# Optimization experiments

Hardware: AMD Instinct MI355X
Metric: run time of the kernel (lower is better)

The kernel has to match this reference:

```python
import jax, jax.numpy as jnp
import numpy as np

B, N, D = 8192, 50, 64


def setup_inputs() -> dict:
    key = jax.random.key(0)
    k1, k2, k3 = jax.random.split(key, 3)
    F = jax.random.normal(k1, (B, N, D), dtype=jnp.float32)
    # xavier_normal for square DxD linear: std = sqrt(2/(D+D)) = 1/sqrt(D)
    std = 1.0 / np.sqrt(D)
    K_w = jax.random.normal(k2, (D, D), dtype=jnp.float32) * std
    Q_w = jax.random.normal(k3, (D, D), dtype=jnp.float32) * std
    return {"F": F, "K_w": K_w, "Q_w": Q_w}


def reference(F, K_w, Q_w):
    # K(F): Linear with weight K_w (torch convention: x @ W^T)
    KF = jnp.einsum('bnd,ed->bne', F, K_w)          # [B,N,D]
    # S = F @ K(F)^T
    S = jnp.einsum('bnd,bmd->bnm', F, KF)           # [B,N,N]
    # out[b,n,d] = sum_m S[b,n,m] * F[b,n,d] * F[b,m,d]
    #            = F[b,n,d] * (S @ F)[b,n,d]   (algebraic fusion of the
    #              bnd,bmd->bnmd outer product + weighted sum over m)
    out = F * jnp.einsum('bnm,bmd->bnd', S, F)      # [B,N,D]
    # residual branch: Q(F)
    out = out + jnp.einsum('bnd,ed->bne', F, Q_w)
    return out
```

## Files before the change

### kernel.cpp

```cpp
#include <hip/hip_runtime.h>

typedef __attribute__((ext_vector_type(8))) short s16x8;
typedef __attribute__((ext_vector_type(4))) short s16x4;
typedef __attribute__((ext_vector_type(4))) float f32x4;

#define ST 72
#define NB 8
#define MFMA __builtin_amdgcn_mfma_f32_16x16x32_bf16

__device__ __forceinline__ short f2bf(float f) {
    unsigned u = __builtin_bit_cast(unsigned, f);
    u += 0x7FFFu + ((u >> 16) & 1u);
    return (short)(u >> 16);
}
__device__ __forceinline__ s16x8 cvt8(f32x4 a, f32x4 b) {
    s16x8 r = { f2bf(a.x), f2bf(a.y), f2bf(a.z), f2bf(a.w),
                f2bf(b.x), f2bf(b.y), f2bf(b.z), f2bf(b.w) };
    return r;
}

__global__ __launch_bounds__(256, 4) void sam3e_v2(
    const float* __restrict__ F, const float* __restrict__ Kw,
    const float* __restrict__ Qw, float* __restrict__ out)
{
    __shared__ __align__(16) short sKw[64 * ST];
    __shared__ __align__(16) short sQw[64 * ST];
    __shared__ __align__(16) short sAT[64 * ST];
    __shared__ __align__(16) short sKS[64 * ST];

    const int tid  = threadIdx.x;
    const int w    = tid >> 6;
    const int lane = tid & 63;
    const int col  = lane & 15;
    const int q    = lane >> 4;

    {
        const int e  = tid & 63;
        const int dg = tid >> 6;
        const f32x4* Kv = (const f32x4*)(Kw + e * 64 + dg * 16);
        const f32x4* Qv = (const f32x4*)(Qw + e * 64 + dg * 16);
        #pragma unroll
        for (int k = 0; k < 4; ++k) {
            f32x4 kv = Kv[k], qv = Qv[k];
            s16x4 hk = { f2bf(kv.x), f2bf(kv.y), f2bf(kv.z), f2bf(kv.w) };
            s16x4 hq = { f2bf(qv.x), f2bf(qv.y), f2bf(qv.z), f2bf(qv.w) };
            *(s16x4*)&sKw[e * ST + dg * 16 + k * 4] = hk;
            *(s16x4*)&sQw[e * ST + dg * 16 + k * 4] = hq;
        }
    }

    const int sn  = tid & 63;
    const int sdg = tid >> 6;
    const f32x4 z4 = {0.f, 0.f, 0.f, 0.f};

    int b = blockIdx.x * NB;
    f32x4 pf0 = z4, pf1 = z4, pf2 = z4, pf3 = z4;
    if (sn < 50) {
        const f32x4* Fr = (const f32x4*)(F + (size_t)b * 3200 + sn * 64 + sdg * 16);
        pf0 = Fr[0]; pf1 = Fr[1]; pf2 = Fr[2]; pf3 = Fr[3];
    }

    for (int it = 0; it < NB; ++it, ++b) {
        const float* Fb = F   + (size_t)b * 3200;
        float*       Ob = out + (size_t)b * 3200;

        __syncthreads();

        {
            const int d0 = sdg * 16;
            short h[16] = { f2bf(pf0.x), f2bf(pf0.y), f2bf(pf0.z), f2bf(pf0.w),
                            f2bf(pf1.x), f2bf(pf1.y), f2bf(pf1.z), f2bf(pf1.w),
                            f2bf(pf2.x), f2bf(pf2.y), f2bf(pf2.z), f2bf(pf2.w),
                            f2bf(pf3.x), f2bf(pf3.y), f2bf(pf3.z), f2bf(pf3.w) };
            #pragma unroll
            for (int i = 0; i < 16; ++i) sAT[(d0 + i) * ST + sn] = h[i];
        }

        s16x8 a0, a1;
        {
            const int row = 16 * w + col;
            f32x4 v0 = z4, v1 = z4, v2 = z4, v3 = z4;
            if (row < 50) {
                const f32x4* Fr = (const f32x4*)(Fb + row * 64);
                v0 = Fr[2 * q]; v1 = Fr[2 * q + 1];
                v2 = Fr[8 + 2 * q]; v3 = Fr[8 + 2 * q + 1];
            }
            a0 = cvt8(v0, v1); a1 = cvt8(v2, v3);
        }

        #pragma unroll
        for (int nt = 0; nt < 4; ++nt) {
            const short* yb = &sKw[(16 * nt + col) * ST + 8 * q];
            f32x4 acc = {0.f, 0.f, 0.f, 0.f};
            acc = MFMA(a0, *(const s16x8*)yb,        acc, 0, 0, 0);
            acc = MFMA(a1, *(const s16x8*)(yb + 32), acc, 0, 0, 0);
            #pragma unroll
            for (int r = 0; r < 4; ++r)
                sKS[(16 * w + 4 * q + r) * ST + 16 * nt + col] = f2bf(acc[r]);
        }
        __syncthreads();

        f32x4 S[4];
        #pragma unroll
        for (int nt = 0; nt < 4; ++nt) {
            const short* yb = &sKS[(16 * nt + col) * ST + 8 * q];
            f32x4 acc = {0.f, 0.f, 0.f, 0.f};
            acc = MFMA(a0, *(const s16x8*)yb,        acc, 0, 0, 0);
            acc = MFMA(a1, *(const s16x8*)(yb + 32), acc, 0, 0, 0);
            S[nt] = acc;
        }

        if (it + 1 < NB && sn < 50) {
            const f32x4* Fr = (const f32x4*)(Fb + 3200 + sn * 64 + sdg * 16);
            pf0 = Fr[0]; pf1 = Fr[1]; pf2 = Fr[2]; pf3 = Fr[3];
        }

        __syncthreads();
        #pragma unroll
        for (int nt = 0; nt < 4; ++nt)
            #pragma unroll
            for (int r = 0; r < 4; ++r)
                sKS[(16 * w + 4 * q + r) * ST + 16 * nt + col] = f2bf(S[nt][r]);
        __syncthreads();

        const short* sb = &sKS[(16 * w + col) * ST + 8 * q];
        s16x8 s0 = *(const s16x8*)sb;
        s16x8 s1 = *(const s16x8*)(sb + 32);
        #pragma unroll
        for (int nt = 0; nt < 4; ++nt) {
            const short* tb = &sAT[(16 * nt + col) * ST + 8 * q];
            const short* qb = &sQw[(16 * nt + col) * ST + 8 * q];
            f32x4 t  = {0.f, 0.f, 0.f, 0.f};
            f32x4 qa = {0.f, 0.f, 0.f, 0.f};
            t  = MFMA(s0, *(const s16x8*)tb,        t,  0, 0, 0);
            t  = MFMA(s1, *(const s16x8*)(tb + 32), t,  0, 0, 0);
            qa = MFMA(a0, *(const s16x8*)qb,        qa, 0, 0, 0);
            qa = MFMA(a1, *(const s16x8*)(qb + 32), qa, 0, 0, 0);
            #pragma unroll
            for (int r = 0; r < 4; ++r) {
                const int n = 16 * w + 4 * q + r;
                if (n < 50) {
                    const int idx = n * 64 + 16 * nt + col;
                    Ob[idx] = Fb[idx] * t[r] + qa[r];
                }
            }
        }
    }
}

extern "C" void kernel_launch(void* const* d_in, const int* in_sizes, int n_in,
                              void* d_out, int out_size, void* d_ws, size_t ws_size,
                              hipStream_t stream) {
    const float* F  = (const float*)d_in[0];
    const float* Kw = (const float*)d_in[1];
    const float* Qw = (const float*)d_in[2];
    float* out = (float*)d_out;
    sam3e_v2<<<8192 / NB, 256, 0, stream>>>(F, Kw, Qw, out);
}
```

Baseline: 237.9 us.

## Give each wavefront its own batch items with private LDS and register-held weights

Restructures the kernel so each wavefront processes whole batch items independently, using a private LDS slice per wave and removing all block-level barriers. K and Q weights are converted to bf16 and kept in registers instead of LDS, the MFMA operand order is transposed so outputs come out as float4-vectorized stores, and the transposed-F LDS layout uses an XOR swizzle to reduce bank conflicts. It drops the previous register prefetch of the next batch item and lowers the occupancy hint, trading barrier stalls for higher register pressure and less latency hiding.

Measured after the change: 232.5 us. -2.2%, faster.

```diff
diff --git a/kernel.cpp b/kernel.cpp
--- a/kernel.cpp
+++ b/kernel.cpp
@@ -5,7 +5,6 @@
 typedef __attribute__((ext_vector_type(4))) float f32x4;
 
 #define ST 72
-#define NB 8
 #define MFMA __builtin_amdgcn_mfma_f32_16x16x32_bf16
 
 __device__ __forceinline__ short f2bf(float f) {
@@ -18,15 +17,16 @@
                 f2bf(b.x), f2bf(b.y), f2bf(b.z), f2bf(b.w) };
     return r;
 }
+__device__ __forceinline__ s16x4 cvt4(f32x4 a) {
+    s16x4 r = { f2bf(a.x), f2bf(a.y), f2bf(a.z), f2bf(a.w) };
+    return r;
+}
 
-__global__ __launch_bounds__(256, 4) void sam3e_v2(
+__global__ __launch_bounds__(256, 2) void sam3e_v3(
     const float* __restrict__ F, const float* __restrict__ Kw,
     const float* __restrict__ Qw, float* __restrict__ out)
 {
-    __shared__ __align__(16) short sKw[64 * ST];
-    __shared__ __align__(16) short sQw[64 * ST];
-    __shared__ __align__(16) short sAT[64 * ST];
-    __shared__ __align__(16) short sKS[64 * ST];
+    __shared__ __align__(16) short lds[4][2][64 * ST];
 
     const int tid  = threadIdx.x;
     const int w    = tid >> 6;
@@ -34,114 +34,110 @@
     const int col  = lane & 15;
     const int q    = lane >> 4;
 
-    {
-        const int e  = tid & 63;
-        const int dg = tid >> 6;
-        const f32x4* Kv = (const f32x4*)(Kw + e * 64 + dg * 16);
-        const f32x4* Qv = (const f32x4*)(Qw + e * 64 + dg * 16);
+    short* sAT = &lds[w][0][0];
+    short* sKS = &lds[w][1][0];
+
+    s16x8 kX[4][2], qX[4][2];
+    #pragma unroll
+    for (int t = 0; t < 4; ++t) {
+        const float* kr = Kw + (16*t + col)*64 + 8*q;
+        const float* qr = Qw + (16*t + col)*64 + 8*q;
         #pragma unroll
-        for (int k = 0; k < 4; ++k) {
-            f32x4 kv = Kv[k], qv = Qv[k];
-            s16x4 hk = { f2bf(kv.x), f2bf(kv.y), f2bf(kv.z), f2bf(kv.w) };
-            s16x4 hq = { f2bf(qv.x), f2bf(qv.y), f2bf(qv.z), f2bf(qv.w) };
-            *(s16x4*)&sKw[e * ST + dg * 16 + k * 4] = hk;
-            *(s16x4*)&sQw[e * ST + dg * 16 + k * 4] = hq;
+        for (int h = 0; h < 2; ++h) {
+            kX[t][h] = cvt8(*(const f32x4*)(kr + 32*h), *(const f32x4*)(kr + 32*h + 4));
+            qX[t][h] = cvt8(*(const f32x4*)(qr + 32*h), *(const f32x4*)(qr + 32*h + 4));
         }
     }
 
-    const int sn  = tid & 63;
-    const int sdg = tid >> 6;
     const f32x4 z4 = {0.f, 0.f, 0.f, 0.f};
+    const int gw = blockIdx.x * 4 + w;
 
-    int b = blockIdx.x * NB;
-    f32x4 pf0 = z4, pf1 = z4, pf2 = z4, pf3 = z4;
-    if (sn < 50) {
-        const f32x4* Fr = (const f32x4*)(F + (size_t)b * 3200 + sn * 64 + sdg * 16);
-        pf0 = Fr[0]; pf1 = Fr[1]; pf2 = Fr[2]; pf3 = Fr[3];
-    }
-
-    for (int it = 0; it < NB; ++it, ++b) {
+    #pragma unroll 1
+    for (int it = 0; it < 4; ++it) {
+        const int b = gw * 4 + it;
         const float* Fb = F   + (size_t)b * 3200;
         float*       Ob = out + (size_t)b * 3200;
 
-        __syncthreads();
-
-        {
-            const int d0 = sdg * 16;
-            short h[16] = { f2bf(pf0.x), f2bf(pf0.y), f2bf(pf0.z), f2bf(pf0.w),
-                            f2bf(pf1.x), f2bf(pf1.y), f2bf(pf1.z), f2bf(pf1.w),
-                            f2bf(pf2.x), f2bf(pf2.y), f2bf(pf2.z), f2bf(pf2.w),
-                            f2bf(pf3.x), f2bf(pf3.y), f2bf(pf3.z), f2bf(pf3.w) };
+        s16x8 aX[4][2];
+        #pragma unroll
+        for (int t = 0; t < 4; ++t) {
+            const int n = 16*t + col;
+            f32x4 v0 = z4, v1 = z4, v2 = z4, v3 = z4;
+            if (n < 50) {
+                const f32x4* Fr = (const f32x4*)(Fb + n*64 + 8*q);
+                v0 = Fr[0]; v1 = Fr[1]; v2 = Fr[8]; v3 = Fr[9];
+            }
+            aX[t][0] = cvt8(v0, v1);
+            aX[t][1] = cvt8(v2, v3);
+            const int mc = n ^ (q << 3);
+            short h0[8] = { f2bf(v0.x), f2bf(v0.y), f2bf(v0.z), f2bf(v0.w),
+                            f2bf(v1.x), f2bf(v1.y), f2bf(v1.z), f2bf(v1.w) };
+            short h1[8] = { f2bf(v2.x), f2bf(v2.y), f2bf(v2.z), f2bf(v2.w),
+                            f2bf(v3.x), f2bf(v3.y), f2bf(v3.z), f2bf(v3.w) };
             #pragma unroll
-            for (int i = 0; i < 16; ++i) sAT[(d0 + i) * ST + sn] = h[i];
-        }
-
-        s16x8 a0, a1;
-        {
-            const int row = 16 * w + col;
-            f32x4 v0 = z4, v1 = z4, v2 = z4, v3 = z4;
-            if (row < 50) {
-                const f32x4* Fr = (const f32x4*)(Fb + row * 64);
-                v0 = Fr[2 * q]; v1 = Fr[2 * q + 1];
-                v2 = Fr[8 + 2 * q]; v3 = Fr[8 + 2 * q + 1];
+            for (int i = 0; i < 8; ++i) {
+                sAT[(8*q + i)*ST + mc]      = h0[i];
+                sAT[(32 + 8*q + i)*ST + mc] = h1[i];
             }
-            a0 = cvt8(v0, v1); a1 = cvt8(v2, v3);
         }
 
         #pragma unroll
-        for (int nt = 0; nt < 4; ++nt) {
-            const short* yb = &sKw[(16 * nt + col) * ST + 8 * q];
-            f32x4 acc = {0.f, 0.f, 0.f, 0.f};
-            acc = MFMA(a0, *(const s16x8*)yb,        acc, 0, 0, 0);
-            acc = MFMA(a1, *(const s16x8*)(yb + 32), acc, 0, 0, 0);
+        for (int et = 0; et < 4; ++et) {
             #pragma unroll
-            for (int r = 0; r < 4; ++r)
-                sKS[(16 * w + 4 * q + r) * ST + 16 * nt + col] = f2bf(acc[r]);
+            for (int nt = 0; nt < 4; ++nt) {
+                f32x4 acc = z4;
+                acc = MFMA(kX[et][0], aX[nt][0], acc, 0, 0, 0);
+                acc = MFMA(kX[et][1], aX[nt][1], acc, 0, 0, 0);
+                *(s16x4*)&sKS[(16*nt + col)*ST + 16*et + 4*q] = cvt4(acc);
+            }
         }
-        __syncthreads();
 
-        f32x4 S[4];
+        s16x8 fK[4][2];
+        #pragma unroll
+        for (int mt = 0; mt < 4; ++mt) {
+            fK[mt][0] = *(const s16x8*)&sKS[(16*mt + col)*ST + 8*q];
+            fK[mt][1] = *(const s16x8*)&sKS[(16*mt + col)*ST + 32 + 8*q];
+        }
+        #pragma unroll
+        for (int mt = 0; mt < 4; ++mt) {
+            #pragma unroll
+            for (int nt = 0; nt < 4; ++nt) {
+                f32x4 acc = z4;
+                acc = MFMA(fK[mt][0], aX[nt][0], acc, 0, 0, 0);
+                acc = MFMA(fK[mt][1], aX[nt][1], acc, 0, 0, 0);
+                *(s16x4*)&sKS[(16*nt + col)*ST + 16*mt + 4*q] = cvt4(acc);
+            }
+        }
+
+        s16x8 yS[4][2];
         #pragma unroll
         for (int nt = 0; nt < 4; ++nt) {
-            const short* yb = &sKS[(16 * nt + col) * ST + 8 * q];
-            f32x4 acc = {0.f, 0.f, 0.f, 0.f};
-            acc = MFMA(a0, *(const s16x8*)yb,        acc, 0, 0, 0);
-            acc = MFMA(a1, *(const s16x8*)(yb + 32), acc, 0, 0, 0);
-            S[nt] = acc;
+            yS[nt][0] = *(const s16x8*)&sKS[(16*nt + col)*ST + 8*q];
+            yS[nt][1] = *(const s16x8*)&sKS[(16*nt + col)*ST + 32 + 8*q];
         }
-
-        if (it + 1 < NB && sn < 50) {
-            const f32x4* Fr = (const f32x4*)(Fb + 3200 + sn * 64 + sdg * 16);
-            pf0 = Fr[0]; pf1 = Fr[1]; pf2 = Fr[2]; pf3 = Fr[3];
-        }
-
-        __syncthreads();
         #pragma unroll
-        for (int nt = 0; nt < 4; ++nt)
+        for (int dt = 0; dt < 4; ++dt) {
+            const int drow = 16*dt + col;
+            const int sw   = (drow >> 3) & 3;
+            const s16x8 xA0 = *(const s16x8*)&sAT[drow*ST + 8*(q ^ sw)];
+            const s16x8 xA1 = *(const s16x8*)&sAT[drow*ST + 8*((q ^ sw) + 4)];
             #pragma unroll
-            for (int r = 0; r < 4; ++r)
-                sKS[(16 * w + 4 * q + r) * ST + 16 * nt + col] = f2bf(S[nt][r]);
-        __syncthreads();
-
-        const short* sb = &sKS[(16 * w + col) * ST + 8 * q];
-        s16x8 s0 = *(const s16x8*)sb;
-        s16x8 s1 = *(const s16x8*)(sb + 32);
-        #pragma unroll
-        for (int nt = 0; nt < 4; ++nt) {
-            const short* tb = &sAT[(16 * nt + col) * ST + 8 * q];
-            const short* qb = &sQw[(16 * nt + col) * ST + 8 * q];
-            f32x4 t  = {0.f, 0.f, 0.f, 0.f};
-            f32x4 qa = {0.f, 0.f, 0.f, 0.f};
-            t  = MFMA(s0, *(const s16x8*)tb,        t,  0, 0, 0);
-            t  = MFMA(s1, *(const s16x8*)(tb + 32), t,  0, 0, 0);
-            qa = MFMA(a0, *(const s16x8*)qb,        qa, 0, 0, 0);
-            qa = MFMA(a1, *(const s16x8*)(qb + 32), qa, 0, 0, 0);
-            #pragma unroll
-            for (int r = 0; r < 4; ++r) {
-                const int n = 16 * w + 4 * q + r;
+            for (int nt = 0; nt < 4; ++nt) {
+                f32x4 tacc = z4, qacc = z4;
+                tacc = MFMA(xA0, yS[nt][0], tacc, 0, 0, 0);
+                tacc = MFMA(xA1, yS[nt][1], tacc, 0, 0, 0);
+                qacc = MFMA(qX[dt][0], aX[nt][0], qacc, 0, 0, 0);
+                qacc = MFMA(qX[dt][1], aX[nt][1], qacc, 0, 0, 0);
+                const int n = 16*nt + col;
                 if (n < 50) {
-                    const int idx = n * 64 + 16 * nt + col;
-                    Ob[idx] = Fb[idx] * t[r] + qa[r];
+                    const int d0 = 16*dt + 4*q;
+                    const f32x4 Fv = *(const f32x4*)(Fb + n*64 + d0);
+                    f32x4 o;
+                    o.x = Fv.x * tacc.x + qacc.x;
+                    o.y = Fv.y * tacc.y + qacc.y;
+                    o.z = Fv.z * tacc.z + qacc.z;
+                    o.w = Fv.w * tacc.w + qacc.w;
+                    *(f32x4*)(Ob + n*64 + d0) = o;
                 }
             }
         }
@@ -155,5 +151,5 @@
     const float* Kw = (const float*)d_in[1];
     const float* Qw = (const float*)d_in[2];
     float* out = (float*)d_out;
-    sam3e_v2<<<8192 / NB, 256, 0, stream>>>(F, Kw, Qw, out);
+    sam3e_v3<<<512, 256, 0, stream>>>(F, Kw, Qw, out);
 }
```
